# Kernel optimization log

Hardware: AMD Instinct MI355X
Metric: run time of the kernel (lower is better)

The kernel has to match this reference:

```python
import jax, jax.numpy as jnp
import numpy as np


def setup_inputs() -> dict:
    key = jax.random.key(0)
    ks = jax.random.split(key, 5)
    B, C, D, H, W = 2, 256, 8, 28, 28
    mid = C // 2
    # Kaiming-normal-ish init (std = sqrt(2/fan_in)) for 1x1 conv weights
    def kaiming(k, shape, fan_in):
        return jax.random.normal(k, shape, dtype=jnp.float32) * np.sqrt(2.0 / fan_in)
    x = jax.random.normal(ks[0], (B, C, D, H, W), dtype=jnp.float32)
    w1 = kaiming(ks[1], (mid, C), C)
    w2 = kaiming(ks[2], (mid, C), C)
    w3 = kaiming(ks[3], (mid, C), C)
    w4 = kaiming(ks[4], (C, mid), mid)
    b1 = jnp.zeros((mid,), jnp.float32)
    b2 = jnp.zeros((mid,), jnp.float32)
    b3 = jnp.zeros((mid,), jnp.float32)
    b4 = jnp.zeros((C,), jnp.float32)
    return {"x": x, "w1": w1, "b1": b1, "w2": w2, "b2": b2,
            "w3": w3, "b3": b3, "w4": w4, "b4": b4}


def reference(x, w1, b1, w2, b2, w3, b3, w4, b4):
    # x: [B, C, D, H, W]; 1x1x1 Conv3d == channel matmul over flattened N = D*H*W
    B, C, D, H, W = x.shape
    N = D * H * W
    xf = x.reshape(B, C, N)                                   # [B, C, N]
    # theta: conv1 -> [B, N, mid]
    e1 = jnp.einsum('mc,bcn->bnm', w1, xf) + b1               # [B, N, mid]
    # phi: conv2 -> [B, mid, N]
    e2 = jnp.einsum('mc,bcn->bmn', w2, xf) + b2[:, None]      # [B, mid, N]
    # g: conv3 -> [B, N, mid]
    e3 = jnp.einsum('mc,bcn->bnm', w3, xf) + b3               # [B, N, mid]
    # unscaled attention: softmax over keys (last axis)
    kernel = jnp.einsum('bnm,bmk->bnk', e1, e2)               # [B, N, N]
    kernel = jax.nn.softmax(kernel, axis=2)
    attn = jnp.einsum('bnk,bkm->bnm', kernel, e3)             # [B, N, mid]
    # conv4 (1x1 Conv1d): mid -> C, applied on [B, mid, N]
    y = jnp.einsum('cm,bnm->bcn', w4, attn) + b4[:, None]     # [B, C, N]
    return x + y.reshape(B, C, D, H, W)
```

## Files before the change

### kernel.cpp

```cpp
#include <hip/hip_runtime.h>


#define BB  2
#define CC  256
#define NN  6272
#define MID 128
#define KS  4
#define QB  128
#define NT  (NN / 64)
#define LOG2E 1.4426950408889634f

typedef _Float16 half2_t __attribute__((ext_vector_type(2)));
typedef _Float16 half4_t __attribute__((ext_vector_type(4)));
typedef _Float16 half8_t __attribute__((ext_vector_type(8)));
typedef float    floatx16 __attribute__((ext_vector_type(16)));
typedef int      i32x2 __attribute__((ext_vector_type(2)));
typedef unsigned u32x4 __attribute__((ext_vector_type(4)));

__device__ __forceinline__ unsigned pkrtz(float a, float b) {
    return __builtin_bit_cast(unsigned, __builtin_amdgcn_cvt_pkrtz(a, b));
}
__device__ __forceinline__ half8_t cvt8(const float* p) {
    float4 f0 = *(const float4*)p;
    float4 f1 = *(const float4*)(p + 4);
    u32x4 u;
    u[0] = pkrtz(f0.x, f0.y); u[1] = pkrtz(f0.z, f0.w);
    u[2] = pkrtz(f1.x, f1.y); u[3] = pkrtz(f1.z, f1.w);
    return __builtin_bit_cast(half8_t, u);
}

__global__ __launch_bounds__(256, 2) void proj_kernel(
    const float* __restrict__ x,
    const float* __restrict__ w1, const float* __restrict__ bi1,
    const float* __restrict__ w2, const float* __restrict__ bi2,
    const float* __restrict__ w3, const float* __restrict__ bi3,
    _Float16* __restrict__ Qg, _Float16* __restrict__ Kg, _Float16* __restrict__ VtG)
{
    const int t    = threadIdx.x;
    const int lane = t & 63;
    const int wave = t >> 6;
    const int l31  = lane & 31;
    const int l5   = lane >> 5;
    const int n0   = blockIdx.x * 64;
    const int b    = blockIdx.y;

    __shared__ _Float16 xhi[64 * 140];
    __shared__ _Float16 xlo[64 * 140];

    floatx16 acc[6];
    #pragma unroll
    for (int i = 0; i < 6; ++i)
        #pragma unroll
        for (int j = 0; j < 16; ++j) acc[i][j] = 0.f;

    for (int phase = 0; phase < 2; ++phase) {
        const int cb = phase * 128;
        if (phase) __syncthreads();
        for (int it = 0; it < 8; ++it) {
            int r = it * 256 + t;
            int c = r >> 4, j4 = (r & 15) << 2;
            float4 v = *(const float4*)(x + ((size_t)b * CC + cb + c) * NN + n0 + j4);
            float vv[4] = {v.x, v.y, v.z, v.w};
            #pragma unroll
            for (int i = 0; i < 4; ++i) {
                _Float16 h = (_Float16)vv[i];
                xhi[(j4 + i) * 140 + c] = h;
                xlo[(j4 + i) * 140 + c] = (_Float16)(vv[i] - (float)h);
            }
        }
        __syncthreads();

        #pragma unroll
        for (int i = 0; i < 6; ++i) {
            const int tau = wave * 6 + i;
            const int pj = tau >> 3, mt = (tau >> 1) & 3, nt = tau & 1;
            const float* w = (pj == 0) ? w1 : (pj == 1) ? w2 : w3;
            const float* wrow = w + (size_t)(mt * 32 + l31) * CC + cb + l5 * 8;
            const _Float16* xr_hi = xhi + (nt * 32 + l31) * 140 + l5 * 8;
            const _Float16* xr_lo = xlo + (nt * 32 + l31) * 140 + l5 * 8;
            #pragma unroll
            for (int ds = 0; ds < 8; ++ds) {
                half8_t wf = cvt8(wrow + ds * 16);
                half8_t ah = *(const half8_t*)(xr_hi + ds * 16);
                half8_t al = *(const half8_t*)(xr_lo + ds * 16);
                if (pj < 2) {
                    acc[i] = __builtin_amdgcn_mfma_f32_32x32x16_f16(ah, wf, acc[i], 0, 0, 0);
                    acc[i] = __builtin_amdgcn_mfma_f32_32x32x16_f16(al, wf, acc[i], 0, 0, 0);
                } else {
                    acc[i] = __builtin_amdgcn_mfma_f32_32x32x16_f16(wf, ah, acc[i], 0, 0, 0);
                    acc[i] = __builtin_amdgcn_mfma_f32_32x32x16_f16(wf, al, acc[i], 0, 0, 0);
                }
            }
        }
    }

    #pragma unroll
    for (int i = 0; i < 6; ++i) {
        const int tau = wave * 6 + i;
        const int pj = tau >> 3, mt = (tau >> 1) & 3, nt = tau & 1;
        if (pj < 2) {
            const float bm = ((pj == 0) ? bi1 : bi2)[mt * 32 + l31];
            const float sc = (pj == 0) ? LOG2E : 1.0f;
            _Float16* eo = ((pj == 0) ? Qg : Kg) + (size_t)b * NN * MID;
            #pragma unroll
            for (int j = 0; j < 16; ++j) {
                int n = n0 + nt * 32 + (j & 3) + 8 * (j >> 2) + 4 * l5;
                eo[(size_t)n * MID + mt * 32 + l31] = (_Float16)((acc[i][j] + bm) * sc);
            }
        } else {
            _Float16* eo = VtG + (size_t)b * MID * NN;
            #pragma unroll
            for (int j = 0; j < 16; ++j) {
                int m = mt * 32 + (j & 3) + 8 * (j >> 2) + 4 * l5;
                eo[(size_t)m * NN + n0 + nt * 32 + l31] = (_Float16)(acc[i][j] + bi3[m]);
            }
        }
    }
}

__global__ __launch_bounds__(256, 2) void attn_kernel(
    const _Float16* __restrict__ Qg, const _Float16* __restrict__ Kg,
    const _Float16* __restrict__ VtG, _Float16* __restrict__ Opart,
    float* __restrict__ MLg)
{
    const int t    = threadIdx.x;
    const int lane = t & 63;
    const int wave = t >> 6;
    const int l31  = lane & 31;
    const int l5   = lane >> 5;
    const int q0   = blockIdx.x * QB;
    const int sp   = blockIdx.y;
    const int b    = blockIdx.z;
    const int kt0  = (NT * sp) / KS;
    const int kt1  = (NT * (sp + 1)) / KS;

    __shared__ __align__(16) char lds[69632];
    _Float16* Ks0 = (_Float16*)lds;
    _Float16* Ks1 = (_Float16*)(lds + 17408);
    _Float16* Vt0 = (_Float16*)(lds + 34816);
    _Float16* Vt1 = (_Float16*)(lds + 52224);
    _Float16* Osh = (_Float16*)lds;

    const _Float16* Qb = Qg + ((size_t)b * NN + q0 + wave * 32) * MID;
    const _Float16* Kb = Kg + (size_t)b * NN * MID;
    const _Float16* Vb = VtG + (size_t)b * MID * NN;

    half8_t qf[8];
    #pragma unroll
    for (int ds = 0; ds < 8; ++ds)
        qf[ds] = *(const half8_t*)(Qb + (size_t)l31 * MID + ds * 16 + l5 * 8);

    floatx16 o[4];
    #pragma unroll
    for (int dt = 0; dt < 4; ++dt)
        #pragma unroll
        for (int j = 0; j < 16; ++j) o[dt][j] = 0.f;
    float m_run = -3.0e38f, l_run = 0.f;

    const int krow_t = t >> 4, koff_t = (t & 15) * 8;
    const int vd_t   = t >> 3, voff_t = (t & 7) * 8;

    #pragma unroll
    for (int it = 0; it < 4; ++it) {
        int r = it * 16 + krow_t;
        *(half8_t*)(Ks0 + r * 136 + koff_t) =
            *(const half8_t*)(Kb + (size_t)(kt0 * 64 + r) * MID + koff_t);
    }
    #pragma unroll
    for (int it = 0; it < 4; ++it) {
        int d = it * 32 + vd_t;
        *(half8_t*)(Vt0 + d * 68 + voff_t) =
            *(const half8_t*)(Vb + (size_t)d * NN + kt0 * 64 + voff_t);
    }
    __syncthreads();

    for (int kt = kt0, cbuf = 0; kt < kt1; ++kt, cbuf ^= 1) {
        const int nk = kt * 64;
        _Float16* KBcur = cbuf ? Ks1 : Ks0;
        _Float16* KBnxt = cbuf ? Ks0 : Ks1;
        _Float16* VBcur = cbuf ? Vt1 : Vt0;
        _Float16* VBnxt = cbuf ? Vt0 : Vt1;

        const int nk2 = (kt + 1 < kt1) ? nk + 64 : nk;
        half8_t vreg[4], kreg[4];
        #pragma unroll
        for (int it = 0; it < 4; ++it)
            vreg[it] = *(const half8_t*)(Vb + (size_t)(it * 32 + vd_t) * NN + nk2 + voff_t);
        #pragma unroll
        for (int it = 0; it < 4; ++it)
            kreg[it] = *(const half8_t*)(Kb + (size_t)(nk2 + it * 16 + krow_t) * MID + koff_t);
        __builtin_amdgcn_sched_barrier(0);

        floatx16 s0, s1;
        #pragma unroll
        for (int j = 0; j < 16; ++j) { s0[j] = 0.f; s1[j] = 0.f; }
        const _Float16* krow0 = KBcur + l31 * 136 + l5 * 8;
        const _Float16* krow1 = KBcur + (32 + l31) * 136 + l5 * 8;
        __builtin_amdgcn_s_setprio(1);
        #pragma unroll
        for (int ds = 0; ds < 8; ++ds) {
            s0 = __builtin_amdgcn_mfma_f32_32x32x16_f16(
                     *(const half8_t*)(krow0 + ds * 16), qf[ds], s0, 0, 0, 0);
            s1 = __builtin_amdgcn_mfma_f32_32x32x16_f16(
                     *(const half8_t*)(krow1 + ds * 16), qf[ds], s1, 0, 0, 0);
        }
        __builtin_amdgcn_s_setprio(0);

        float tmax = fmaxf(s0[0], s1[0]);
        #pragma unroll
        for (int j = 1; j < 16; ++j) tmax = fmaxf(tmax, fmaxf(s0[j], s1[j]));
        tmax = fmaxf(tmax, __shfl_xor(tmax, 32));

        if (!__all(tmax <= m_run)) {
            const float m_new = fmaxf(m_run, tmax);
            const float alpha = exp2f(m_run - m_new);
            m_run = m_new;
            l_run *= alpha;
            #pragma unroll
            for (int dt = 0; dt < 4; ++dt)
                #pragma unroll
                for (int j = 0; j < 16; ++j) o[dt][j] *= alpha;
        }

        float psum = 0.f;
        unsigned u0[8], u1[8];
        #pragma unroll
        for (int g = 0; g < 4; ++g) {
            float p0 = exp2f(s0[4 * g + 0] - m_run);
            float p1 = exp2f(s0[4 * g + 1] - m_run);
            float p2 = exp2f(s0[4 * g + 2] - m_run);
            float p3 = exp2f(s0[4 * g + 3] - m_run);
            psum += (p0 + p1) + (p2 + p3);
            u0[g] = pkrtz(p0, p1);
            u1[g] = pkrtz(p2, p3);
        }
        #pragma unroll
        for (int g = 0; g < 4; ++g) {
            float p0 = exp2f(s1[4 * g + 0] - m_run);
            float p1 = exp2f(s1[4 * g + 1] - m_run);
            float p2 = exp2f(s1[4 * g + 2] - m_run);
            float p3 = exp2f(s1[4 * g + 3] - m_run);
            psum += (p0 + p1) + (p2 + p3);
            u0[4 + g] = pkrtz(p0, p1);
            u1[4 + g] = pkrtz(p2, p3);
        }
        psum += __shfl_xor(psum, 32);
        l_run += psum;

        #pragma unroll
        for (int it = 0; it < 4; ++it)
            *(half8_t*)(VBnxt + (it * 32 + vd_t) * 68 + voff_t) = vreg[it];
        #pragma unroll
        for (int it = 0; it < 4; ++it)
            *(half8_t*)(KBnxt + (it * 16 + krow_t) * 136 + koff_t) = kreg[it];

        __builtin_amdgcn_s_setprio(1);
        #pragma unroll
        for (int ks = 0; ks < 4; ++ks) {
            i32x2 rA = __builtin_amdgcn_permlane32_swap(
                           (int)u0[2 * ks], (int)u0[2 * ks + 1], false, false);
            i32x2 rB = __builtin_amdgcn_permlane32_swap(
                           (int)u1[2 * ks], (int)u1[2 * ks + 1], false, false);
            u32x4 pw;
            pw[0] = (unsigned)rA[0]; pw[1] = (unsigned)rB[0];
            pw[2] = (unsigned)rA[1]; pw[3] = (unsigned)rB[1];
            half8_t pf = __builtin_bit_cast(half8_t, pw);
            const _Float16* vcol = VBcur + ks * 16 + l5 * 8;
            #pragma unroll
            for (int dt = 0; dt < 4; ++dt)
                o[dt] = __builtin_amdgcn_mfma_f32_32x32x16_f16(
                            *(const half8_t*)(vcol + (dt * 32 + l31) * 68), pf,
                            o[dt], 0, 0, 0);
        }
        __builtin_amdgcn_s_setprio(0);

        __syncthreads();
    }

    if (l5 == 0) {
        float* mlb = MLg + ((size_t)(b * KS + sp) * 2) * NN;
        mlb[q0 + wave * 32 + l31]      = m_run;
        mlb[NN + q0 + wave * 32 + l31] = l_run;
    }

    #pragma unroll
    for (int dt = 0; dt < 4; ++dt)
        #pragma unroll
        for (int h = 0; h < 4; ++h) {
            half4_t v;
            #pragma unroll
            for (int i = 0; i < 4; ++i) v[i] = (_Float16)o[dt][4 * h + i];
            *(half4_t*)(Osh + (wave * 32 + l31) * 136 + dt * 32 + 8 * h + 4 * l5) = v;
        }
    __syncthreads();
    _Float16* Ob = Opart + ((size_t)(b * KS + sp) * NN + q0) * MID;
    #pragma unroll
    for (int it = 0; it < 8; ++it) {
        int c = it * 256 + t;
        int q = c >> 4, g = c & 15;
        *(half8_t*)(Ob + (size_t)q * MID + g * 8) =
            *(const half8_t*)(Osh + q * 136 + g * 8);
    }
}

__global__ __launch_bounds__(256, 4) void comb_kernel(
    const _Float16* __restrict__ Opart, const float* __restrict__ MLg,
    _Float16* __restrict__ attnW)
{
    const int t  = threadIdx.x;
    const int b  = blockIdx.y;
    const int q  = blockIdx.x * 32 + (t >> 3);
    const int dg = (t & 7) * 16;

    float mv[KS], lv[KS];
    float m_g = -3.0e38f;
    #pragma unroll
    for (int s = 0; s < KS; ++s) {
        const float* mlb = MLg + ((size_t)(b * KS + s) * 2) * NN;
        mv[s] = mlb[q];
        lv[s] = mlb[NN + q];
        m_g = fmaxf(m_g, mv[s]);
    }
    float lg = 0.f, w[KS];
    #pragma unroll
    for (int s = 0; s < KS; ++s) { w[s] = exp2f(mv[s] - m_g); lg += lv[s] * w[s]; }
    const float inv = 1.0f / lg;

    float acc[16];
    #pragma unroll
    for (int j = 0; j < 16; ++j) acc[j] = 0.f;
    #pragma unroll
    for (int s = 0; s < KS; ++s) {
        const half8_t* Op = (const half8_t*)(Opart + ((size_t)(b * KS + s) * NN + q) * MID + dg);
        half8_t v0 = Op[0], v1 = Op[1];
        #pragma unroll
        for (int j = 0; j < 8; ++j) {
            acc[j]     += (float)v0[j] * w[s];
            acc[8 + j] += (float)v1[j] * w[s];
        }
    }
    half8_t h0, h1;
    #pragma unroll
    for (int j = 0; j < 8; ++j) {
        h0[j] = (_Float16)(acc[j] * inv);
        h1[j] = (_Float16)(acc[8 + j] * inv);
    }
    half8_t* Ow = (half8_t*)(attnW + ((size_t)b * NN + q) * MID + dg);
    Ow[0] = h0; Ow[1] = h1;
}

__global__ __launch_bounds__(256, 2) void epi_kernel(
    const _Float16* __restrict__ attnW, const float* __restrict__ w4,
    const float* __restrict__ b4, const float* __restrict__ x,
    float* __restrict__ out)
{
    const int t    = threadIdx.x;
    const int lane = t & 63;
    const int wave = t >> 6;
    const int l31  = lane & 31;
    const int l5   = lane >> 5;
    const int n0   = blockIdx.x * 64;
    const int b    = blockIdx.y;

    #pragma unroll
    for (int i = 0; i < 4; ++i) {
        const int tau = wave * 4 + i;
        const int ct = tau >> 1, nt = tau & 1;
        floatx16 acc;
        #pragma unroll
        for (int j = 0; j < 16; ++j) acc[j] = 0.f;

        const float* wrow = w4 + (size_t)(ct * 32 + l31) * MID + l5 * 8;
        const _Float16* brow = attnW + ((size_t)b * NN + n0 + nt * 32 + l31) * MID + l5 * 8;
        #pragma unroll
        for (int ds = 0; ds < 8; ++ds) {
            half8_t wf = cvt8(wrow + ds * 16);
            half8_t bf = *(const half8_t*)(brow + ds * 16);
            acc = __builtin_amdgcn_mfma_f32_32x32x16_f16(wf, bf, acc, 0, 0, 0);
        }
        #pragma unroll
        for (int j = 0; j < 16; ++j) {
            int c = ct * 32 + (j & 3) + 8 * (j >> 2) + 4 * l5;
            size_t off = ((size_t)b * CC + c) * NN + n0 + nt * 32 + l31;
            out[off] = acc[j] + b4[c] + x[off];
        }
    }
}

extern "C" void kernel_launch(void* const* d_in, const int* in_sizes, int n_in,
                              void* d_out, int out_size, void* d_ws, size_t ws_size,
                              hipStream_t stream)
{
    const float* x  = (const float*)d_in[0];
    const float* w1 = (const float*)d_in[1];
    const float* b1 = (const float*)d_in[2];
    const float* w2 = (const float*)d_in[3];
    const float* b2 = (const float*)d_in[4];
    const float* w3 = (const float*)d_in[5];
    const float* b3 = (const float*)d_in[6];
    const float* w4 = (const float*)d_in[7];
    const float* b4 = (const float*)d_in[8];
    float* out = (float*)d_out;

    _Float16* Qg    = (_Float16*)d_ws;
    _Float16* Kg    = Qg + (size_t)BB * NN * MID;
    _Float16* VtG   = Kg + (size_t)BB * NN * MID;
    _Float16* attnW = VtG + (size_t)BB * NN * MID;
    float* MLg      = (float*)(attnW + (size_t)BB * NN * MID);
    _Float16* Opart = (_Float16*)d_out;

    proj_kernel<<<dim3(NN / 64, BB), 256, 0, stream>>>(x, w1, b1, w2, b2, w3, b3, Qg, Kg, VtG);
    attn_kernel<<<dim3(NN / QB, KS, BB), 256, 0, stream>>>(Qg, Kg, VtG, Opart, MLg);
    comb_kernel<<<dim3(NN / 32, BB), 256, 0, stream>>>(Opart, MLg, attnW);
    epi_kernel<<<dim3(NN / 64, BB), 256, 0, stream>>>(attnW, w4, b4, x, out);
}
```

Baseline: 290.5 us.

## Software-pipeline QK^T and softmax-PV across iterations; vectorize x staging writes

The attention loop is restructured so the QK^T MFMAs for tile kt run before the softmax and PV of tile kt-1. This lets matrix work and exp/VALU work from different tiles overlap, and the V tile is now loaded one iteration later than K. Separately, the x-to-LDS hi/lo fp16 split in the projection kernel now loads four channel rows per thread and writes half4 vectors instead of scalar halves. The pipelining keeps an extra pair of score accumulators live, which raises register pressure, and it adds an epilogue step plus an extra barrier.

```diff
diff --git a/kernel.cpp b/kernel.cpp
--- a/kernel.cpp
+++ b/kernel.cpp
@@ -56,16 +56,28 @@
     for (int phase = 0; phase < 2; ++phase) {
         const int cb = phase * 128;
         if (phase) __syncthreads();
-        for (int it = 0; it < 8; ++it) {
-            int r = it * 256 + t;
-            int c = r >> 4, j4 = (r & 15) << 2;
-            float4 v = *(const float4*)(x + ((size_t)b * CC + cb + c) * NN + n0 + j4);
-            float vv[4] = {v.x, v.y, v.z, v.w};
-            #pragma unroll
-            for (int i = 0; i < 4; ++i) {
-                _Float16 h = (_Float16)vv[i];
-                xhi[(j4 + i) * 140 + c] = h;
-                xlo[(j4 + i) * 140 + c] = (_Float16)(vv[i] - (float)h);
+        #pragma unroll
+        for (int a = t; a < 512; a += 256) {
+            int cg = a >> 4, ng = a & 15;
+            int c  = cg * 4, n4 = ng * 4;
+            const float* xb = x + ((size_t)b * CC + cb + c) * NN + n0 + n4;
+            float4 v0 = *(const float4*)(xb);
+            float4 v1 = *(const float4*)(xb + NN);
+            float4 v2 = *(const float4*)(xb + 2 * (size_t)NN);
+            float4 v3 = *(const float4*)(xb + 3 * (size_t)NN);
+            const float* pv[4] = {&v0.x, &v1.x, &v2.x, &v3.x};
+            #pragma unroll
+            for (int nn = 0; nn < 4; ++nn) {
+                half4_t h, l;
+                #pragma unroll
+                for (int ci = 0; ci < 4; ++ci) {
+                    float f = pv[ci][nn];
+                    _Float16 hh = (_Float16)f;
+                    h[ci] = hh;
+                    l[ci] = (_Float16)(f - (float)hh);
+                }
+                *(half4_t*)&xhi[(n4 + nn) * 140 + c] = h;
+                *(half4_t*)&xlo[(n4 + nn) * 140 + c] = l;
             }
         }
         __syncthreads();
@@ -160,55 +172,10 @@
     const int krow_t = t >> 4, koff_t = (t & 15) * 8;
     const int vd_t   = t >> 3, voff_t = (t & 7) * 8;
 
-    #pragma unroll
-    for (int it = 0; it < 4; ++it) {
-        int r = it * 16 + krow_t;
-        *(half8_t*)(Ks0 + r * 136 + koff_t) =
-            *(const half8_t*)(Kb + (size_t)(kt0 * 64 + r) * MID + koff_t);
-    }
-    #pragma unroll
-    for (int it = 0; it < 4; ++it) {
-        int d = it * 32 + vd_t;
-        *(half8_t*)(Vt0 + d * 68 + voff_t) =
-            *(const half8_t*)(Vb + (size_t)d * NN + kt0 * 64 + voff_t);
-    }
-    __syncthreads();
-
-    for (int kt = kt0, cbuf = 0; kt < kt1; ++kt, cbuf ^= 1) {
-        const int nk = kt * 64;
-        _Float16* KBcur = cbuf ? Ks1 : Ks0;
-        _Float16* KBnxt = cbuf ? Ks0 : Ks1;
-        _Float16* VBcur = cbuf ? Vt1 : Vt0;
-        _Float16* VBnxt = cbuf ? Vt0 : Vt1;
-
-        const int nk2 = (kt + 1 < kt1) ? nk + 64 : nk;
-        half8_t vreg[4], kreg[4];
-        #pragma unroll
-        for (int it = 0; it < 4; ++it)
-            vreg[it] = *(const half8_t*)(Vb + (size_t)(it * 32 + vd_t) * NN + nk2 + voff_t);
-        #pragma unroll
-        for (int it = 0; it < 4; ++it)
-            kreg[it] = *(const half8_t*)(Kb + (size_t)(nk2 + it * 16 + krow_t) * MID + koff_t);
-        __builtin_amdgcn_sched_barrier(0);
-
-        floatx16 s0, s1;
-        #pragma unroll
-        for (int j = 0; j < 16; ++j) { s0[j] = 0.f; s1[j] = 0.f; }
-        const _Float16* krow0 = KBcur + l31 * 136 + l5 * 8;
-        const _Float16* krow1 = KBcur + (32 + l31) * 136 + l5 * 8;
-        __builtin_amdgcn_s_setprio(1);
-        #pragma unroll
-        for (int ds = 0; ds < 8; ++ds) {
-            s0 = __builtin_amdgcn_mfma_f32_32x32x16_f16(
-                     *(const half8_t*)(krow0 + ds * 16), qf[ds], s0, 0, 0, 0);
-            s1 = __builtin_amdgcn_mfma_f32_32x32x16_f16(
-                     *(const half8_t*)(krow1 + ds * 16), qf[ds], s1, 0, 0, 0);
-        }
-        __builtin_amdgcn_s_setprio(0);
-
-        float tmax = fmaxf(s0[0], s1[0]);
-        #pragma unroll
-        for (int j = 1; j < 16; ++j) tmax = fmaxf(tmax, fmaxf(s0[j], s1[j]));
+    auto smpv = [&](const floatx16& p0, const floatx16& p1, const _Float16* VB) {
+        float tmax = fmaxf(p0[0], p1[0]);
+        #pragma unroll
+        for (int j = 1; j < 16; ++j) tmax = fmaxf(tmax, fmaxf(p0[j], p1[j]));
         tmax = fmaxf(tmax, __shfl_xor(tmax, 32));
 
         if (!__all(tmax <= m_run)) {
@@ -226,33 +193,26 @@
         unsigned u0[8], u1[8];
         #pragma unroll
         for (int g = 0; g < 4; ++g) {
-            float p0 = exp2f(s0[4 * g + 0] - m_run);
-            float p1 = exp2f(s0[4 * g + 1] - m_run);
-            float p2 = exp2f(s0[4 * g + 2] - m_run);
-            float p3 = exp2f(s0[4 * g + 3] - m_run);
-            psum += (p0 + p1) + (p2 + p3);
-            u0[g] = pkrtz(p0, p1);
-            u1[g] = pkrtz(p2, p3);
+            float e0 = exp2f(p0[4 * g + 0] - m_run);
+            float e1 = exp2f(p0[4 * g + 1] - m_run);
+            float e2 = exp2f(p0[4 * g + 2] - m_run);
+            float e3 = exp2f(p0[4 * g + 3] - m_run);
+            psum += (e0 + e1) + (e2 + e3);
+            u0[g] = pkrtz(e0, e1);
+            u1[g] = pkrtz(e2, e3);
         }
         #pragma unroll
         for (int g = 0; g < 4; ++g) {
-            float p0 = exp2f(s1[4 * g + 0] - m_run);
-            float p1 = exp2f(s1[4 * g + 1] - m_run);
-            float p2 = exp2f(s1[4 * g + 2] - m_run);
-            float p3 = exp2f(s1[4 * g + 3] - m_run);
-            psum += (p0 + p1) + (p2 + p3);
-            u0[4 + g] = pkrtz(p0, p1);
-            u1[4 + g] = pkrtz(p2, p3);
+            float e0 = exp2f(p1[4 * g + 0] - m_run);
+            float e1 = exp2f(p1[4 * g + 1] - m_run);
+            float e2 = exp2f(p1[4 * g + 2] - m_run);
+            float e3 = exp2f(p1[4 * g + 3] - m_run);
+            psum += (e0 + e1) + (e2 + e3);
+            u0[4 + g] = pkrtz(e0, e1);
+            u1[4 + g] = pkrtz(e2, e3);
         }
         psum += __shfl_xor(psum, 32);
         l_run += psum;
-
-        #pragma unroll
-        for (int it = 0; it < 4; ++it)
-            *(half8_t*)(VBnxt + (it * 32 + vd_t) * 68 + voff_t) = vreg[it];
-        #pragma unroll
-        for (int it = 0; it < 4; ++it)
-            *(half8_t*)(KBnxt + (it * 16 + krow_t) * 136 + koff_t) = kreg[it];
 
         __builtin_amdgcn_s_setprio(1);
         #pragma unroll
@@ -265,7 +225,7 @@
             pw[0] = (unsigned)rA[0]; pw[1] = (unsigned)rB[0];
             pw[2] = (unsigned)rA[1]; pw[3] = (unsigned)rB[1];
             half8_t pf = __builtin_bit_cast(half8_t, pw);
-            const _Float16* vcol = VBcur + ks * 16 + l5 * 8;
+            const _Float16* vcol = VB + ks * 16 + l5 * 8;
             #pragma unroll
             for (int dt = 0; dt < 4; ++dt)
                 o[dt] = __builtin_amdgcn_mfma_f32_32x32x16_f16(
@@ -273,8 +233,65 @@
                             o[dt], 0, 0, 0);
         }
         __builtin_amdgcn_s_setprio(0);
-
+    };
+
+    #pragma unroll
+    for (int it = 0; it < 4; ++it) {
+        int r = it * 16 + krow_t;
+        *(half8_t*)(Ks0 + r * 136 + koff_t) =
+            *(const half8_t*)(Kb + (size_t)(kt0 * 64 + r) * MID + koff_t);
+    }
+    __syncthreads();
+
+    floatx16 sp0, sp1;
+    for (int kt = kt0, cbuf = 0; kt < kt1; ++kt, cbuf ^= 1) {
+        const int nk = kt * 64;
+        _Float16* KBcur = cbuf ? Ks1 : Ks0;
+        _Float16* KBnxt = cbuf ? Ks0 : Ks1;
+        _Float16* VBcur = cbuf ? Vt1 : Vt0;
+        _Float16* VBnxt = cbuf ? Vt0 : Vt1;
+
+        const int nk2 = (kt + 1 < kt1) ? nk + 64 : nk;
+        half8_t vreg[4], kreg[4];
+        #pragma unroll
+        for (int it = 0; it < 4; ++it)
+            vreg[it] = *(const half8_t*)(Vb + (size_t)(it * 32 + vd_t) * NN + nk + voff_t);
+        #pragma unroll
+        for (int it = 0; it < 4; ++it)
+            kreg[it] = *(const half8_t*)(Kb + (size_t)(nk2 + it * 16 + krow_t) * MID + koff_t);
+        __builtin_amdgcn_sched_barrier(0);
+
+        floatx16 s0, s1;
+        #pragma unroll
+        for (int j = 0; j < 16; ++j) { s0[j] = 0.f; s1[j] = 0.f; }
+        const _Float16* krow0 = KBcur + l31 * 136 + l5 * 8;
+        const _Float16* krow1 = KBcur + (32 + l31) * 136 + l5 * 8;
+        __builtin_amdgcn_s_setprio(1);
+        #pragma unroll
+        for (int ds = 0; ds < 8; ++ds) {
+            s0 = __builtin_amdgcn_mfma_f32_32x32x16_f16(
+                     *(const half8_t*)(krow0 + ds * 16), qf[ds], s0, 0, 0, 0);
+            s1 = __builtin_amdgcn_mfma_f32_32x32x16_f16(
+                     *(const half8_t*)(krow1 + ds * 16), qf[ds], s1, 0, 0, 0);
+        }
+        __builtin_amdgcn_s_setprio(0);
+
+        if (kt > kt0) smpv(sp0, sp1, VBcur);
+
+        #pragma unroll
+        for (int it = 0; it < 4; ++it)
+            *(half8_t*)(VBnxt + (it * 32 + vd_t) * 68 + voff_t) = vreg[it];
+        #pragma unroll
+        for (int it = 0; it < 4; ++it)
+            *(half8_t*)(KBnxt + (it * 16 + krow_t) * 136 + koff_t) = kreg[it];
+
+        sp0 = s0; sp1 = s1;
         __syncthreads();
+    }
+
+    {
+        const int cbE = (kt1 - kt0) & 1;
+        smpv(sp0, sp1, cbE ? Vt1 : Vt0);
     }
 
     if (l5 == 0) {
@@ -282,7 +299,7 @@
         mlb[q0 + wave * 32 + l31]      = m_run;
         mlb[NN + q0 + wave * 32 + l31] = l_run;
     }
-
+    __syncthreads();
     #pragma unroll
     for (int dt = 0; dt < 4; ++dt)
         #pragma unroll
```

Result: no change. 287.1 us (-1.2%).
